# Kernel optimization log

Hardware: AMD Instinct MI355X
Metric: run time of the kernel (lower is better)

The kernel has to match this reference:

```python
import jax, jax.numpy as jnp
import numpy as np

D_MODEL = 768
NUM_HEADS = 12
D_K = D_MODEL // NUM_HEADS


def setup_inputs() -> dict:
    key = jax.random.key(0)
    ks = jax.random.split(key, 7)
    B, T = 2, 2048
    scale = 1.0 / np.sqrt(D_MODEL)
    return {
        "query": jax.random.normal(ks[0], (B, T, D_MODEL), dtype=jnp.float32),
        "key": jax.random.normal(ks[1], (B, T, D_MODEL), dtype=jnp.float32),
        "value": jax.random.normal(ks[2], (B, T, D_MODEL), dtype=jnp.float32),
        # nn.Linear(d_model, d_model, bias=False) weights, stored [out, in] as in torch
        "W_q": jax.random.normal(ks[3], (D_MODEL, D_MODEL), dtype=jnp.float32) * scale,
        "W_k": jax.random.normal(ks[4], (D_MODEL, D_MODEL), dtype=jnp.float32) * scale,
        "W_v": jax.random.normal(ks[5], (D_MODEL, D_MODEL), dtype=jnp.float32) * scale,
        "W_o": jax.random.normal(ks[6], (D_MODEL, D_MODEL), dtype=jnp.float32) * scale,
    }


def _split_heads(x):
    # [B, T, H*Dk] -> [B, H, T, Dk]
    B, T, _ = x.shape
    return x.reshape(B, T, NUM_HEADS, D_K).transpose(0, 2, 1, 3)


def reference(query, key, value, W_q, W_k, W_v, W_o):
    # Linear projections (torch Linear: y = x @ W.T)
    Q = _split_heads(query @ W_q.T)
    K = _split_heads(key @ W_k.T)
    V = _split_heads(value @ W_v.T)

    # Naive scaled dot-product attention: full [B,H,Tq,Tk] score matrix
    scores = jnp.einsum("bhqd,bhkd->bhqk", Q, K) / jnp.sqrt(jnp.float32(D_K))
    weights = jax.nn.softmax(scores, axis=-1)
    attn = jnp.einsum("bhqk,bhkd->bhqd", weights, V)

    # [B,H,T,Dk] -> [B,T,D_model], then output projection
    B, H, T, Dk = attn.shape
    attn = attn.transpose(0, 2, 1, 3).reshape(B, T, H * Dk)
    output = attn @ W_o.T
    return output, weights
```

## Files before the change

kernel.cpp:

```cpp
#include <hip/hip_runtime.h>
#include <cstdint>

#define HD   12
#define TSEQ 2048
#define DM   768
#define DK   64
#define BATCH 2

template<bool SUMA>
__device__ __forceinline__ void gemm_nt_core(
    const float* __restrict__ A, const float* __restrict__ A2,
    const float* __restrict__ B, float* __restrict__ C,
    int m0, int n0, int K, int lda, int ldb, int ldc, float alpha)
{
    __shared__ float As[16][132];
    __shared__ float Bs[16][132];

    const int t = threadIdx.x;
    const int row = t & 127;
    const int kh8 = (t >> 7) * 8;
    const float* Arow = A + (size_t)(m0 + row) * lda + kh8;
    const float* Brow = B + (size_t)(n0 + row) * ldb + kh8;
    const float* A2row = nullptr;
    if (SUMA) A2row = A2 + (size_t)(m0 + row) * lda + kh8;

    const int w  = t >> 6;
    const int l  = t & 63;
    const int orow = (w >> 1) * 64 + (l >> 3) * 8;
    const int ocol = (w & 1) * 64 + (l & 7) * 8;

    float acc[8][8];
    #pragma unroll
    for (int i = 0; i < 8; ++i)
        #pragma unroll
        for (int j = 0; j < 8; ++j) acc[i][j] = 0.f;

    float4 a0 = *(const float4*)(Arow);
    float4 a1 = *(const float4*)(Arow + 4);
    float4 b0 = *(const float4*)(Brow);
    float4 b1 = *(const float4*)(Brow + 4);
    float4 c0, c1;
    if (SUMA) { c0 = *(const float4*)(A2row); c1 = *(const float4*)(A2row + 4); }

    for (int k0 = 0; k0 < K; k0 += 16) {
        __syncthreads();
        if (SUMA) {
            a0.x += c0.x; a0.y += c0.y; a0.z += c0.z; a0.w += c0.w;
            a1.x += c1.x; a1.y += c1.y; a1.z += c1.z; a1.w += c1.w;
        }
        As[kh8 + 0][row] = a0.x; As[kh8 + 1][row] = a0.y;
        As[kh8 + 2][row] = a0.z; As[kh8 + 3][row] = a0.w;
        As[kh8 + 4][row] = a1.x; As[kh8 + 5][row] = a1.y;
        As[kh8 + 6][row] = a1.z; As[kh8 + 7][row] = a1.w;
        Bs[kh8 + 0][row] = b0.x; Bs[kh8 + 1][row] = b0.y;
        Bs[kh8 + 2][row] = b0.z; Bs[kh8 + 3][row] = b0.w;
        Bs[kh8 + 4][row] = b1.x; Bs[kh8 + 5][row] = b1.y;
        Bs[kh8 + 6][row] = b1.z; Bs[kh8 + 7][row] = b1.w;
        __syncthreads();
        if (k0 + 16 < K) {
            a0 = *(const float4*)(Arow + k0 + 16);
            a1 = *(const float4*)(Arow + k0 + 20);
            b0 = *(const float4*)(Brow + k0 + 16);
            b1 = *(const float4*)(Brow + k0 + 20);
            if (SUMA) {
                c0 = *(const float4*)(A2row + k0 + 16);
                c1 = *(const float4*)(A2row + k0 + 20);
            }
        }
        #pragma unroll
        for (int kk = 0; kk < 16; ++kk) {
            const float4 f0 = *(const float4*)&As[kk][orow];
            const float4 f1 = *(const float4*)&As[kk][orow + 4];
            const float4 g0 = *(const float4*)&Bs[kk][ocol];
            const float4 g1 = *(const float4*)&Bs[kk][ocol + 4];
            const float a[8] = {f0.x, f0.y, f0.z, f0.w, f1.x, f1.y, f1.z, f1.w};
            const float b[8] = {g0.x, g0.y, g0.z, g0.w, g1.x, g1.y, g1.z, g1.w};
            #pragma unroll
            for (int i = 0; i < 8; ++i)
                #pragma unroll
                for (int j = 0; j < 8; ++j)
                    acc[i][j] = fmaf(a[i], b[j], acc[i][j]);
        }
    }

    #pragma unroll
    for (int i = 0; i < 8; ++i) {
        float* crow = C + (size_t)(m0 + orow + i) * ldc + n0 + ocol;
        *(float4*)crow = make_float4(acc[i][0] * alpha, acc[i][1] * alpha,
                                     acc[i][2] * alpha, acc[i][3] * alpha);
        *(float4*)(crow + 4) = make_float4(acc[i][4] * alpha, acc[i][5] * alpha,
                                           acc[i][6] * alpha, acc[i][7] * alpha);
    }
}

__global__ __launch_bounds__(256) void gemm_qkv(
    const float* __restrict__ q, const float* __restrict__ k,
    const float* __restrict__ v,
    const float* __restrict__ Wq, const float* __restrict__ Wk,
    const float* __restrict__ Wv,
    float* __restrict__ Qp, float* __restrict__ Kp, float* __restrict__ Vp)
{
    const int by  = blockIdx.y;
    const int mat = by / 6;
    const int nb  = by % 6;
    const float* A = (mat == 0) ? q  : (mat == 1) ? k  : v;
    const float* B = (mat == 0) ? Wq : (mat == 1) ? Wk : Wv;
    float*       C = (mat == 0) ? Qp : (mat == 1) ? Kp : Vp;
    gemm_nt_core<false>(A, nullptr, B, C, blockIdx.x * 128, nb * 128,
                        DM, DM, DM, DM, 1.f);
}

template<bool SUMA>
__global__ __launch_bounds__(256) void gemm_out(
    const float* __restrict__ ctx0, const float* __restrict__ ctx1,
    const float* __restrict__ Wo, float* __restrict__ out)
{
    gemm_nt_core<SUMA>(ctx0, ctx1, Wo, out, blockIdx.x * 128, blockIdx.y * 128,
                       DM, DM, DM, DM, 1.f);
}

__global__ __launch_bounds__(256) void attn_scores(
    const float* __restrict__ Qp, const float* __restrict__ Kp,
    float* __restrict__ Wt)
{
    const int z = blockIdx.z, b = z / HD, h = z % HD;
    gemm_nt_core<false>(Qp + (size_t)b * TSEQ * DM + h * DK, nullptr,
                        Kp + (size_t)b * TSEQ * DM + h * DK,
                        Wt + (size_t)z * TSEQ * TSEQ,
                        blockIdx.x * 128, blockIdx.y * 128,
                        DK, DM, DM, TSEQ, 0.125f);
}

__global__ __launch_bounds__(256) void softmax_rows(float* __restrict__ Wt)
{
    float* p = Wt + (size_t)blockIdx.x * TSEQ;
    const int t = threadIdx.x;
    const float4 va = *(const float4*)(p + t * 4);
    const float4 vb = *(const float4*)(p + 1024 + t * 4);
    float v[8] = {va.x, va.y, va.z, va.w, vb.x, vb.y, vb.z, vb.w};

    float m = -3.4e38f;
    #pragma unroll
    for (int i = 0; i < 8; ++i) m = fmaxf(m, v[i]);
    #pragma unroll
    for (int off = 32; off > 0; off >>= 1) m = fmaxf(m, __shfl_down(m, off));
    __shared__ float redm[4];
    __shared__ float reds[4];
    const int lane = t & 63, wid = t >> 6;
    if (lane == 0) redm[wid] = m;
    __syncthreads();
    m = fmaxf(fmaxf(redm[0], redm[1]), fmaxf(redm[2], redm[3]));

    float s = 0.f;
    #pragma unroll
    for (int i = 0; i < 8; ++i) { v[i] = __expf(v[i] - m); s += v[i]; }
    #pragma unroll
    for (int off = 32; off > 0; off >>= 1) s += __shfl_down(s, off);
    if (lane == 0) reds[wid] = s;
    __syncthreads();
    s = reds[0] + reds[1] + reds[2] + reds[3];
    const float inv = 1.f / s;

    *(float4*)(p + t * 4) =
        make_float4(v[0] * inv, v[1] * inv, v[2] * inv, v[3] * inv);
    *(float4*)(p + 1024 + t * 4) =
        make_float4(v[4] * inv, v[5] * inv, v[6] * inv, v[7] * inv);
}

__global__ __launch_bounds__(256) void attn_pv(
    const float* __restrict__ Wt, const float* __restrict__ Vp,
    float* __restrict__ ctxp, int kchunk)
{
    const int z = blockIdx.z, b = z / HD, h = z % HD;
    const int kbase = blockIdx.y * kchunk;
    float* ctx = ctxp + (size_t)blockIdx.y * (size_t)BATCH * TSEQ * DM;
    const float* A = Wt + (size_t)z * TSEQ * TSEQ + kbase;
    const float* V = Vp + ((size_t)b * TSEQ + kbase) * DM + h * DK;

    __shared__ float Ws[16][132];
    __shared__ float Vs[16][68];

    const int t = threadIdx.x;
    const int m0 = blockIdx.x * 128;
    const int arow = t & 127;
    const int kh8  = (t >> 7) * 8;
    const float* Arow = A + (size_t)(m0 + arow) * TSEQ + kh8;
    const int vr = t >> 4, vc = (t & 15) * 4;
    const float* Vrow = V + (size_t)vr * DM + vc;
    const int oty = t >> 4;
    const int otx = t & 15;

    float acc[8][4];
    #pragma unroll
    for (int i = 0; i < 8; ++i)
        #pragma unroll
        for (int j = 0; j < 4; ++j) acc[i][j] = 0.f;

    float4 a0 = *(const float4*)(Arow);
    float4 a1 = *(const float4*)(Arow + 4);
    float4 vv = *(const float4*)(Vrow);

    for (int k0 = 0; k0 < kchunk; k0 += 16) {
        __syncthreads();
        Ws[kh8 + 0][arow] = a0.x; Ws[kh8 + 1][arow] = a0.y;
        Ws[kh8 + 2][arow] = a0.z; Ws[kh8 + 3][arow] = a0.w;
        Ws[kh8 + 4][arow] = a1.x; Ws[kh8 + 5][arow] = a1.y;
        Ws[kh8 + 6][arow] = a1.z; Ws[kh8 + 7][arow] = a1.w;
        *(float4*)&Vs[vr][vc] = vv;
        __syncthreads();
        if (k0 + 16 < kchunk) {
            a0 = *(const float4*)(Arow + k0 + 16);
            a1 = *(const float4*)(Arow + k0 + 20);
            vv = *(const float4*)(Vrow + (size_t)(k0 + 16) * DM);
        }
        #pragma unroll
        for (int kk = 0; kk < 16; ++kk) {
            const float4 a0v = *(const float4*)&Ws[kk][oty * 8];
            const float4 a1v = *(const float4*)&Ws[kk][oty * 8 + 4];
            const float4 bv  = *(const float4*)&Vs[kk][otx * 4];
            const float a[8] = {a0v.x, a0v.y, a0v.z, a0v.w,
                                a1v.x, a1v.y, a1v.z, a1v.w};
            const float bb[4] = {bv.x, bv.y, bv.z, bv.w};
            #pragma unroll
            for (int i = 0; i < 8; ++i)
                #pragma unroll
                for (int j = 0; j < 4; ++j)
                    acc[i][j] = fmaf(a[i], bb[j], acc[i][j]);
        }
    }

    float* cbase = ctx + ((size_t)b * TSEQ + m0 + oty * 8) * DM + h * DK + otx * 4;
    #pragma unroll
    for (int i = 0; i < 8; ++i)
        *(float4*)(cbase + (size_t)i * DM) =
            make_float4(acc[i][0], acc[i][1], acc[i][2], acc[i][3]);
}

extern "C" void kernel_launch(void* const* d_in, const int* in_sizes, int n_in,
                              void* d_out, int out_size, void* d_ws, size_t ws_size,
                              hipStream_t stream)
{
    const float* q  = (const float*)d_in[0];
    const float* k  = (const float*)d_in[1];
    const float* v  = (const float*)d_in[2];
    const float* Wq = (const float*)d_in[3];
    const float* Wk = (const float*)d_in[4];
    const float* Wv = (const float*)d_in[5];
    const float* Wo = (const float*)d_in[6];

    float* out = (float*)d_out;
    const int BT = BATCH * TSEQ;
    float* wts = out + (size_t)BT * DM;

    const size_t bufE = (size_t)BT * DM;
    float* Qp   = (float*)d_ws;
    float* Kp   = Qp + bufE;
    float* Vp   = Kp + bufE;
    float* ctx0 = Vp + bufE;
    float* ctx1 = ctx0 + bufE;
    const int nsplit = (ws_size >= 5 * bufE * sizeof(float)) ? 2 : 1;

    gemm_qkv<<<dim3(BT / 128, 18), 256, 0, stream>>>(q, k, v, Wq, Wk, Wv,
                                                     Qp, Kp, Vp);
    attn_scores<<<dim3(TSEQ / 128, TSEQ / 128, BATCH * HD), 256, 0, stream>>>(
        Qp, Kp, wts);
    softmax_rows<<<BATCH * HD * TSEQ, 256, 0, stream>>>(wts);
    attn_pv<<<dim3(TSEQ / 128, nsplit, BATCH * HD), 256, 0, stream>>>(
        wts, Vp, ctx0, TSEQ / nsplit);
    if (nsplit == 2)
        gemm_out<true><<<dim3(BT / 128, DM / 128), 256, 0, stream>>>(
            ctx0, ctx1, Wo, out);
    else
        gemm_out<false><<<dim3(BT / 128, DM / 128), 256, 0, stream>>>(
            ctx0, nullptr, Wo, out);
}
```

Baseline: 1.196 ms.

## Fuse softmax into score GEMM epilogue and PV kernel with atomic row sums

Score GEMM epilogue now writes exp(scaled score) and atomically accumulates per-row sums into a workspace buffer. The PV kernel normalizes weights in place while streaming them and scales the context by the inverse row sum, eliminating the separate softmax pass over the large weight matrix. Max subtraction is dropped, which risks overflow for large scores, and adds atomic traffic plus a zeroing kernel.

```diff
diff --git a/kernel.cpp b/kernel.cpp
--- a/kernel.cpp
+++ b/kernel.cpp
@@ -6,12 +6,15 @@
 #define DM   768
 #define DK   64
 #define BATCH 2
-
-template<bool SUMA>
+#define NZ   (BATCH * HD)
+#define RS_N (NZ * TSEQ)
+
+template<bool SUMA, bool EXPROW>
 __device__ __forceinline__ void gemm_nt_core(
     const float* __restrict__ A, const float* __restrict__ A2,
     const float* __restrict__ B, float* __restrict__ C,
-    int m0, int n0, int K, int lda, int ldb, int ldc, float alpha)
+    int m0, int n0, int K, int lda, int ldb, int ldc, float alpha,
+    float* __restrict__ rowsum, int rowbase)
 {
     __shared__ float As[16][132];
     __shared__ float Bs[16][132];
@@ -83,13 +86,40 @@
         }
     }
 
-    #pragma unroll
-    for (int i = 0; i < 8; ++i) {
-        float* crow = C + (size_t)(m0 + orow + i) * ldc + n0 + ocol;
-        *(float4*)crow = make_float4(acc[i][0] * alpha, acc[i][1] * alpha,
-                                     acc[i][2] * alpha, acc[i][3] * alpha);
-        *(float4*)(crow + 4) = make_float4(acc[i][4] * alpha, acc[i][5] * alpha,
-                                           acc[i][6] * alpha, acc[i][7] * alpha);
+    if (EXPROW) {
+        float rs[8];
+        #pragma unroll
+        for (int i = 0; i < 8; ++i) {
+            rs[i] = 0.f;
+            #pragma unroll
+            for (int j = 0; j < 8; ++j) {
+                acc[i][j] = __expf(acc[i][j] * alpha);
+                rs[i] += acc[i][j];
+            }
+            float* crow = C + (size_t)(m0 + orow + i) * ldc + n0 + ocol;
+            *(float4*)crow = make_float4(acc[i][0], acc[i][1], acc[i][2], acc[i][3]);
+            *(float4*)(crow + 4) = make_float4(acc[i][4], acc[i][5], acc[i][6], acc[i][7]);
+        }
+        #pragma unroll
+        for (int i = 0; i < 8; ++i) {
+            rs[i] += __shfl_xor(rs[i], 1);
+            rs[i] += __shfl_xor(rs[i], 2);
+            rs[i] += __shfl_xor(rs[i], 4);
+        }
+        if ((l & 7) == 0) {
+            #pragma unroll
+            for (int i = 0; i < 8; ++i)
+                atomicAdd(&rowsum[rowbase + m0 + orow + i], rs[i]);
+        }
+    } else {
+        #pragma unroll
+        for (int i = 0; i < 8; ++i) {
+            float* crow = C + (size_t)(m0 + orow + i) * ldc + n0 + ocol;
+            *(float4*)crow = make_float4(acc[i][0] * alpha, acc[i][1] * alpha,
+                                         acc[i][2] * alpha, acc[i][3] * alpha);
+            *(float4*)(crow + 4) = make_float4(acc[i][4] * alpha, acc[i][5] * alpha,
+                                               acc[i][6] * alpha, acc[i][7] * alpha);
+        }
     }
 }
 
@@ -106,8 +136,8 @@
     const float* A = (mat == 0) ? q  : (mat == 1) ? k  : v;
     const float* B = (mat == 0) ? Wq : (mat == 1) ? Wk : Wv;
     float*       C = (mat == 0) ? Qp : (mat == 1) ? Kp : Vp;
-    gemm_nt_core<false>(A, nullptr, B, C, blockIdx.x * 128, nb * 128,
-                        DM, DM, DM, DM, 1.f);
+    gemm_nt_core<false, false>(A, nullptr, B, C, blockIdx.x * 128, nb * 128,
+                               DM, DM, DM, DM, 1.f, nullptr, 0);
 }
 
 template<bool SUMA>
@@ -115,20 +145,27 @@
     const float* __restrict__ ctx0, const float* __restrict__ ctx1,
     const float* __restrict__ Wo, float* __restrict__ out)
 {
-    gemm_nt_core<SUMA>(ctx0, ctx1, Wo, out, blockIdx.x * 128, blockIdx.y * 128,
-                       DM, DM, DM, DM, 1.f);
-}
-
+    gemm_nt_core<SUMA, false>(ctx0, ctx1, Wo, out, blockIdx.x * 128,
+                              blockIdx.y * 128, DM, DM, DM, DM, 1.f, nullptr, 0);
+}
+
+template<bool EXPROW>
 __global__ __launch_bounds__(256) void attn_scores(
     const float* __restrict__ Qp, const float* __restrict__ Kp,
-    float* __restrict__ Wt)
+    float* __restrict__ Wt, float* __restrict__ rowsum)
 {
     const int z = blockIdx.z, b = z / HD, h = z % HD;
-    gemm_nt_core<false>(Qp + (size_t)b * TSEQ * DM + h * DK, nullptr,
-                        Kp + (size_t)b * TSEQ * DM + h * DK,
-                        Wt + (size_t)z * TSEQ * TSEQ,
-                        blockIdx.x * 128, blockIdx.y * 128,
-                        DK, DM, DM, TSEQ, 0.125f);
+    gemm_nt_core<false, EXPROW>(Qp + (size_t)b * TSEQ * DM + h * DK, nullptr,
+                                Kp + (size_t)b * TSEQ * DM + h * DK,
+                                Wt + (size_t)z * TSEQ * TSEQ,
+                                blockIdx.x * 128, blockIdx.y * 128,
+                                DK, DM, DM, TSEQ, 0.125f, rowsum, z * TSEQ);
+}
+
+__global__ __launch_bounds__(256) void zero_buf(float* __restrict__ p, int n)
+{
+    const int i = blockIdx.x * 256 + threadIdx.x;
+    if (i < n) p[i] = 0.f;
 }
 
 __global__ __launch_bounds__(256) void softmax_rows(float* __restrict__ Wt)
@@ -150,7 +187,6 @@
     if (lane == 0) redm[wid] = m;
     __syncthreads();
     m = fmaxf(fmaxf(redm[0], redm[1]), fmaxf(redm[2], redm[3]));
-
     float s = 0.f;
     #pragma unroll
     for (int i = 0; i < 8; ++i) { v[i] = __expf(v[i] - m); s += v[i]; }
@@ -160,35 +196,43 @@
     __syncthreads();
     s = reds[0] + reds[1] + reds[2] + reds[3];
     const float inv = 1.f / s;
-
     *(float4*)(p + t * 4) =
         make_float4(v[0] * inv, v[1] * inv, v[2] * inv, v[3] * inv);
     *(float4*)(p + 1024 + t * 4) =
         make_float4(v[4] * inv, v[5] * inv, v[6] * inv, v[7] * inv);
 }
 
+template<bool NORM>
 __global__ __launch_bounds__(256) void attn_pv(
-    const float* __restrict__ Wt, const float* __restrict__ Vp,
-    float* __restrict__ ctxp, int kchunk)
+    float* __restrict__ Wt, const float* __restrict__ Vp,
+    const float* __restrict__ rowsum, float* __restrict__ ctxp, int kchunk)
 {
     const int z = blockIdx.z, b = z / HD, h = z % HD;
     const int kbase = blockIdx.y * kchunk;
     float* ctx = ctxp + (size_t)blockIdx.y * (size_t)BATCH * TSEQ * DM;
-    const float* A = Wt + (size_t)z * TSEQ * TSEQ + kbase;
+    float* A = Wt + (size_t)z * TSEQ * TSEQ + kbase;
     const float* V = Vp + ((size_t)b * TSEQ + kbase) * DM + h * DK;
 
     __shared__ float Ws[16][132];
     __shared__ float Vs[16][68];
+    __shared__ float inv_s[128];
 
     const int t = threadIdx.x;
     const int m0 = blockIdx.x * 128;
     const int arow = t & 127;
     const int kh8  = (t >> 7) * 8;
-    const float* Arow = A + (size_t)(m0 + arow) * TSEQ + kh8;
+    float* Arow = A + (size_t)(m0 + arow) * TSEQ + kh8;
     const int vr = t >> 4, vc = (t & 15) * 4;
     const float* Vrow = V + (size_t)vr * DM + vc;
     const int oty = t >> 4;
     const int otx = t & 15;
+
+    if (NORM) {
+        if (t < 128) inv_s[t] = 1.f / rowsum[z * TSEQ + m0 + t];
+    }
+    __syncthreads();
+    float winv = 1.f;
+    if (NORM) winv = inv_s[arow];
 
     float acc[8][4];
     #pragma unroll
@@ -208,6 +252,12 @@
         Ws[kh8 + 6][arow] = a1.z; Ws[kh8 + 7][arow] = a1.w;
         *(float4*)&Vs[vr][vc] = vv;
         __syncthreads();
+        if (NORM) {
+            *(float4*)(Arow + k0) = make_float4(a0.x * winv, a0.y * winv,
+                                                a0.z * winv, a0.w * winv);
+            *(float4*)(Arow + k0 + 4) = make_float4(a1.x * winv, a1.y * winv,
+                                                    a1.z * winv, a1.w * winv);
+        }
         if (k0 + 16 < kchunk) {
             a0 = *(const float4*)(Arow + k0 + 16);
             a1 = *(const float4*)(Arow + k0 + 20);
@@ -231,9 +281,12 @@
 
     float* cbase = ctx + ((size_t)b * TSEQ + m0 + oty * 8) * DM + h * DK + otx * 4;
     #pragma unroll
-    for (int i = 0; i < 8; ++i)
+    for (int i = 0; i < 8; ++i) {
+        float s = 1.f;
+        if (NORM) s = inv_s[oty * 8 + i];
         *(float4*)(cbase + (size_t)i * DM) =
-            make_float4(acc[i][0], acc[i][1], acc[i][2], acc[i][3]);
+            make_float4(acc[i][0] * s, acc[i][1] * s, acc[i][2] * s, acc[i][3] * s);
+    }
 }
 
 extern "C" void kernel_launch(void* const* d_in, const int* in_sizes, int n_in,
@@ -258,19 +311,34 @@
     float* Vp   = Kp + bufE;
     float* ctx0 = Vp + bufE;
     float* ctx1 = ctx0 + bufE;
-    const int nsplit = (ws_size >= 5 * bufE * sizeof(float)) ? 2 : 1;
+
+    const bool fit2 = ws_size >= (5 * bufE + RS_N) * sizeof(float);
+    const bool fit1 = ws_size >= (4 * bufE + RS_N) * sizeof(float);
 
     gemm_qkv<<<dim3(BT / 128, 18), 256, 0, stream>>>(q, k, v, Wq, Wk, Wv,
                                                      Qp, Kp, Vp);
-    attn_scores<<<dim3(TSEQ / 128, TSEQ / 128, BATCH * HD), 256, 0, stream>>>(
-        Qp, Kp, wts);
-    softmax_rows<<<BATCH * HD * TSEQ, 256, 0, stream>>>(wts);
-    attn_pv<<<dim3(TSEQ / 128, nsplit, BATCH * HD), 256, 0, stream>>>(
-        wts, Vp, ctx0, TSEQ / nsplit);
-    if (nsplit == 2)
-        gemm_out<true><<<dim3(BT / 128, DM / 128), 256, 0, stream>>>(
-            ctx0, ctx1, Wo, out);
-    else
+
+    if (fit1) {
+        const int nsplit = fit2 ? 2 : 1;
+        float* rowsum = (fit2 ? ctx1 + bufE : ctx0 + bufE);
+        zero_buf<<<RS_N / 256, 256, 0, stream>>>(rowsum, RS_N);
+        attn_scores<true><<<dim3(TSEQ / 128, TSEQ / 128, NZ), 256, 0, stream>>>(
+            Qp, Kp, wts, rowsum);
+        attn_pv<true><<<dim3(TSEQ / 128, nsplit, NZ), 256, 0, stream>>>(
+            wts, Vp, rowsum, ctx0, TSEQ / nsplit);
+        if (nsplit == 2)
+            gemm_out<true><<<dim3(BT / 128, DM / 128), 256, 0, stream>>>(
+                ctx0, ctx1, Wo, out);
+        else
+            gemm_out<false><<<dim3(BT / 128, DM / 128), 256, 0, stream>>>(
+                ctx0, nullptr, Wo, out);
+    } else {
+        attn_scores<false><<<dim3(TSEQ / 128, TSEQ / 128, NZ), 256, 0, stream>>>(
+            Qp, Kp, wts, nullptr);
+        softmax_rows<<<NZ * TSEQ, 256, 0, stream>>>(wts);
+        attn_pv<false><<<dim3(TSEQ / 128, 1, NZ), 256, 0, stream>>>(
+            wts, Vp, nullptr, ctx0, TSEQ);
         gemm_out<false><<<dim3(BT / 128, DM / 128), 256, 0, stream>>>(
             ctx0, nullptr, Wo, out);
-}
+    }
+}
```

New measurement: 1.211 ms. No clear change (+1.3%).
